# Performance work log

Measured on AMD Instinct MI355X. Metric: run time of the kernel, lower is better.

The kernel has to match this reference:

```python
import jax, jax.numpy as jnp
import numpy as np

D, N, K = 128, 8192, 256


def setup_inputs() -> dict:
    key = jax.random.key(0)
    k1, k2, k3 = jax.random.split(key, 3)
    X = jax.random.normal(k1, (D, N), dtype=jnp.float32)
    N_A = jax.random.normal(k2, (D, D, K), dtype=jnp.float32) / np.sqrt(D)
    N_mu = jax.random.normal(k3, (D, K), dtype=jnp.float32)
    gamma = jnp.float32(-0.01)
    return {"X": X, "N_A": N_A, "N_mu": N_mu, "gamma": gamma}


def reference(X, N_A, N_mu, gamma):
    # N_eval[d,n,c] = sum_e N_A[d,e,c] * (X[e,n] - N_mu[e,c])
    # Split to avoid materializing the (D,D,N,k) broadcast intermediate:
    AX = jnp.einsum('dec,en->dnc', N_A, X)            # (D, N, K)
    Amu = jnp.einsum('dec,ec->dc', N_A, N_mu)          # (D, K)
    N_eval = AX - Amu[:, None, :]                      # (D, N, K)
    sq = jnp.sum(N_eval * N_eval, axis=0)              # (N, K)
    Pi = jax.nn.softmax(gamma * sq, axis=1).T          # (K, N)
    return jnp.vstack((X, Pi))                         # (D+K, N)
```

## Files before the change

kernel.cpp:

```cpp
#include <hip/hip_runtime.h>

#define D_ 128
#define N_ 8192
#define K_ 256

typedef __attribute__((ext_vector_type(4))) float f4;
typedef __attribute__((ext_vector_type(8))) int i8v;
typedef __attribute__((ext_vector_type(4))) int i4v;

__global__ __launch_bounds__(256) void prep_k(
    const float* __restrict__ X, float* __restrict__ out,
    unsigned char* __restrict__ Xf8, const float* __restrict__ NA,
    unsigned char* __restrict__ Af8s, const float* __restrict__ Nmu,
    float* __restrict__ Amut) {
  __shared__ __align__(16) char smem[21568];
  const int t = threadIdx.x;
  const int id = blockIdx.x;

  if (id < 256) {
    float (*tile)[65] = (float (*)[65])smem;
    const int n0 = (id & 127) * 64;
    const int e0 = (id >> 7) * 64;
    const int col = t & 63;
    const int r4 = t >> 6;
    for (int rr = 0; rr < 64; rr += 4) {
      int e = rr + r4;
      float v = X[(size_t)(e0 + e) * N_ + n0 + col];
      tile[e][col] = v;
      out[(size_t)(e0 + e) * N_ + n0 + col] = v;
    }
    __syncthreads();
    const int chunk = t & 15;
    for (int iter = 0; iter < 4; ++iter) {
      int nl = iter * 16 + (t >> 4);
      float v0 = tile[chunk * 4 + 0][nl];
      float v1 = tile[chunk * 4 + 1][nl];
      float v2 = tile[chunk * 4 + 2][nl];
      float v3 = tile[chunk * 4 + 3][nl];
      int pk = __builtin_amdgcn_cvt_pk_fp8_f32(v0, v1, 0, false);
      pk = __builtin_amdgcn_cvt_pk_fp8_f32(v2, v3, pk, true);
      *(int*)&Xf8[(size_t)(n0 + nl) * D_ + e0 + chunk * 4] = pk;
    }
  } else {
    const int aid = id - 256;
    const int dtl = aid & 7;
    const int c0 = (aid >> 3) * 8;
    unsigned char* AT = (unsigned char*)smem;
    float* mu_s = (float*)(smem + 17472);
    {
      const int cl = t & 7;
      const int er = t >> 3;
#pragma unroll
      for (int pass = 0; pass < 4; ++pass) {
        int e = pass * 32 + er;
        mu_s[cl * 128 + e] = Nmu[(size_t)e * K_ + c0 + cl];
      }
    }
    const int c4 = t & 1;
    const int pe = t >> 1;
#pragma unroll 4
    for (int iter = 0; iter < 16; ++iter) {
      int p = iter * 128 + pe;
      int d = p >> 7, e = p & 127;
      float4 v = *(const float4*)&NA[((size_t)(dtl * 16 + d) * D_ + e) * K_ + c0 + c4 * 4];
      int pk0 = __builtin_amdgcn_cvt_pk_fp8_f32(v.x, v.x, 0, false);
      int pk1 = __builtin_amdgcn_cvt_pk_fp8_f32(v.y, v.y, 0, false);
      int pk2 = __builtin_amdgcn_cvt_pk_fp8_f32(v.z, v.z, 0, false);
      int pk3 = __builtin_amdgcn_cvt_pk_fp8_f32(v.w, v.w, 0, false);
      AT[(c4 * 4 + 0) * 2184 + d * 136 + e] = (unsigned char)(pk0 & 0xff);
      AT[(c4 * 4 + 1) * 2184 + d * 136 + e] = (unsigned char)(pk1 & 0xff);
      AT[(c4 * 4 + 2) * 2184 + d * 136 + e] = (unsigned char)(pk2 & 0xff);
      AT[(c4 * 4 + 3) * 2184 + d * 136 + e] = (unsigned char)(pk3 & 0xff);
    }
    __syncthreads();
    if (t < 128) {
      const int d_loc = t >> 3;
      const int cl = t & 7;
      const unsigned char* row = &AT[cl * 2184 + d_loc * 136];
      const float* mr = &mu_s[cl * 128];
      float s = 0.f;
#pragma unroll
      for (int j = 0; j < 16; ++j) {
        int2 v = *(const int2*)(row + j * 8);
        const int e0 = j * 8;
        s += __builtin_amdgcn_cvt_f32_fp8(v.x, 0) * mr[e0 + 0];
        s += __builtin_amdgcn_cvt_f32_fp8(v.x, 1) * mr[e0 + 1];
        s += __builtin_amdgcn_cvt_f32_fp8(v.x, 2) * mr[e0 + 2];
        s += __builtin_amdgcn_cvt_f32_fp8(v.x, 3) * mr[e0 + 3];
        s += __builtin_amdgcn_cvt_f32_fp8(v.y, 0) * mr[e0 + 4];
        s += __builtin_amdgcn_cvt_f32_fp8(v.y, 1) * mr[e0 + 5];
        s += __builtin_amdgcn_cvt_f32_fp8(v.y, 2) * mr[e0 + 6];
        s += __builtin_amdgcn_cvt_f32_fp8(v.y, 3) * mr[e0 + 7];
      }
      Amut[(size_t)(c0 + cl) * D_ + dtl * 16 + d_loc] = -s;
    }
    const int w = t >> 6, L = t & 63, q = L >> 4, m = L & 15;
#pragma unroll
    for (int it = 0; it < 4; ++it) {
      int u = w + it * 4;
      int ucl = u >> 1, h = u & 1;
      const unsigned char* base = AT + ucl * 2184 + m * 136 + q * 32 + h * 16;
      unsigned long long lo = *(const unsigned long long*)(base);
      unsigned long long hi = *(const unsigned long long*)(base + 8);
      ulonglong2 val; val.x = lo; val.y = hi;
      *(ulonglong2*)(Af8s + (size_t)(c0 + ucl) * 16384 + dtl * 2048 + h * 1024 + L * 16) = val;
    }
  }
}

__global__ __launch_bounds__(256, 4) void main_k(
    const unsigned char* __restrict__ Af8s, const unsigned char* __restrict__ Xf8,
    const float* __restrict__ Amut, float* __restrict__ sqws) {
  __shared__ unsigned char A0s[16384];
  __shared__ unsigned char A1s[16384];
  __shared__ float amus[2][D_];
  const int t = threadIdx.x;
  const int w = t >> 6;
  const int L = t & 63;
  const int m = L & 15;
  const int q = L >> 4;

  const int id = blockIdx.x;
  const int xcd = id & 7;
  const int s = id >> 3;
  const int yb = xcd * 4 + (s & 3);
  const int xb = s >> 2;
  const int n0 = xb * 256;
  const int c0 = yb * 8;

  i8v xf[4];
#pragma unroll
  for (int jt = 0; jt < 4; ++jt)
    xf[jt] = *(const i8v*)(Xf8 + (size_t)(n0 + w * 64 + jt * 16 + m) * D_ + q * 32);

  const unsigned char* pl = Af8s + (size_t)c0 * 16384;

#define STAGE(SRC, DST)                                                          \
  {                                                                              \
    _Pragma("unroll")                                                            \
    for (int it_ = 0; it_ < 4; ++it_)                                            \
      __builtin_amdgcn_global_load_lds(                                          \
          (const unsigned int*)((SRC) + (it_ * 256 + t) * 16),                   \
          (unsigned int*)((DST) + (it_ * 256 + w * 64) * 16), 16, 0, 0);         \
  }

  STAGE(pl, A0s);
  if (t < 32)
    __builtin_amdgcn_global_load_lds((const unsigned int*)(Amut + (size_t)c0 * D_ + t * 4),
                                     (unsigned int*)&amus[0][0], 16, 0, 0);

  auto compute = [&](const unsigned char* buf, const float* amurow, int c) {
    float ss0 = 0.f, ss1 = 0.f, ss2 = 0.f, ss3 = 0.f;
#pragma unroll
    for (int dtl = 0; dtl < 8; ++dtl) {
      i4v lo = *(const i4v*)(buf + dtl * 2048 + L * 16);
      i4v hi = *(const i4v*)(buf + dtl * 2048 + 1024 + L * 16);
      i8v a;
      a[0] = lo[0]; a[1] = lo[1]; a[2] = lo[2]; a[3] = lo[3];
      a[4] = hi[0]; a[5] = hi[1]; a[6] = hi[2]; a[7] = hi[3];
      f4 camu = *(const f4*)&amurow[dtl * 16 + q * 4];
#pragma unroll
      for (int jt = 0; jt < 4; ++jt) {
        f4 acc = __builtin_amdgcn_mfma_scale_f32_16x16x128_f8f6f4(
            a, xf[jt], camu, 0, 0, 0, 0x7f7f7f7f, 0, 0x7f7f7f7f);
        float sj = acc[0] * acc[0] + acc[1] * acc[1] + acc[2] * acc[2] + acc[3] * acc[3];
        if (jt == 0) ss0 += sj; else if (jt == 1) ss1 += sj;
        else if (jt == 2) ss2 += sj; else ss3 += sj;
      }
    }
    ss0 += __shfl_xor(ss0, 16, 64);  ss0 += __shfl_xor(ss0, 32, 64);
    ss1 += __shfl_xor(ss1, 16, 64);  ss1 += __shfl_xor(ss1, 32, 64);
    ss2 += __shfl_xor(ss2, 16, 64);  ss2 += __shfl_xor(ss2, 32, 64);
    ss3 += __shfl_xor(ss3, 16, 64);  ss3 += __shfl_xor(ss3, 32, 64);
    float sel = (q == 0) ? ss0 : (q == 1) ? ss1 : (q == 2) ? ss2 : ss3;
    sqws[(size_t)c * N_ + n0 + w * 64 + L] = sel;
  };

  for (int ci2 = 0; ci2 < 4; ++ci2) {
    const int cA = c0 + ci2 * 2;
    __syncthreads();
    STAGE(pl + (size_t)(ci2 * 2 + 1) * 16384, A1s);
    if (t < 32)
      __builtin_amdgcn_global_load_lds(
          (const unsigned int*)(Amut + (size_t)(cA + 1) * D_ + t * 4),
          (unsigned int*)&amus[1][0], 16, 0, 0);
    compute(A0s, &amus[0][0], cA);

    __syncthreads();
    if (ci2 < 3) {
      STAGE(pl + (size_t)(ci2 * 2 + 2) * 16384, A0s);
      if (t < 32)
        __builtin_amdgcn_global_load_lds(
            (const unsigned int*)(Amut + (size_t)(cA + 2) * D_ + t * 4),
            (unsigned int*)&amus[0][0], 16, 0, 0);
    }
    compute(A1s, &amus[1][0], cA + 1);
  }
#undef STAGE
}

__global__ __launch_bounds__(256) void softmax_k(const float* __restrict__ sqws,
                                                 const float* __restrict__ gptr,
                                                 float* __restrict__ out) {
  __shared__ float s_ld[256][36];
  __shared__ float red[8][32];
  __shared__ float red2[8][32];
  const int t = threadIdx.x;
  const int n0 = blockIdx.x * 32;
  const float gamma = *gptr;
#pragma unroll
  for (int it = 0; it < 8; ++it) {
    int f = it * 256 + t;
    int c = f >> 3, nq = f & 7;
    *(float4*)&s_ld[c][nq * 4] = *(const float4*)&sqws[(size_t)c * N_ + n0 + nq * 4];
  }
  __syncthreads();
  const int nl = t & 31;
  const int cg = t >> 5;
  float mxp = -1e30f;
#pragma unroll
  for (int cc = 0; cc < 32; ++cc)
    mxp = fmaxf(mxp, gamma * s_ld[cg * 32 + cc][nl]);
  red[cg][nl] = mxp;
  __syncthreads();
  float mx = red[0][nl];
#pragma unroll
  for (int g2 = 1; g2 < 8; ++g2) mx = fmaxf(mx, red[g2][nl]);
  float ex[32];
  float z = 0.f;
#pragma unroll
  for (int cc = 0; cc < 32; ++cc) {
    ex[cc] = __expf(gamma * s_ld[cg * 32 + cc][nl] - mx);
    z += ex[cc];
  }
  red2[cg][nl] = z;
  __syncthreads();
  float zz = red2[0][nl];
#pragma unroll
  for (int g2 = 1; g2 < 8; ++g2) zz += red2[g2][nl];
  float rz = 1.f / zz;
#pragma unroll
  for (int cc = 0; cc < 32; ++cc)
    out[(size_t)(D_ + cg * 32 + cc) * N_ + n0 + nl] = ex[cc] * rz;
}

extern "C" void kernel_launch(void* const* d_in, const int* in_sizes, int n_in,
                              void* d_out, int out_size, void* d_ws, size_t ws_size,
                              hipStream_t stream) {
  const float* X   = (const float*)d_in[0];
  const float* NA  = (const float*)d_in[1];
  const float* Nmu = (const float*)d_in[2];
  const float* g   = (const float*)d_in[3];
  float* out = (float*)d_out;
  char* ws = (char*)d_ws;

  unsigned char* Xf8  = (unsigned char*)(ws);
  unsigned char* Af8s = (unsigned char*)(ws + 1048576);
  float* Amut         = (float*)(ws + 5242880);
  float* sqws         = (float*)(ws + 5373952);

  hipLaunchKernelGGL(prep_k, dim3(512), dim3(256), 0, stream,
                     X, out, Xf8, NA, Af8s, Nmu, Amut);
  hipLaunchKernelGGL(main_k, dim3(1024), dim3(256), 0, stream,
                     Af8s, Xf8, Amut, sqws);
  hipLaunchKernelGGL(softmax_k, dim3(N_ / 32), dim3(256), 0, stream, sqws, g, out);
}
```

Measured before the change: 114.3 us.

## Switch MFMA operands from FP8 to packed FP6 with custom encoding

Replaces FP8 quantization of X and N_A with a hand-written FP6 (e2m3) encoder. Operands are bit-packed at 6 bits per element, and the MFMA scale instruction runs in FP6 mode. N_A is pre-scaled by 8 and gamma is divided by 64 to compensate. This cuts the workspace and LDS staging bytes for the A planes and X rows, and may allow a faster FP6 MFMA rate. The cost is lower precision with saturation at 7.5, plus extra ALU work for software encoding in the prep kernel.

```diff
diff --git a/kernel.cpp b/kernel.cpp
--- a/kernel.cpp
+++ b/kernel.cpp
@@ -8,10 +8,32 @@
 typedef __attribute__((ext_vector_type(8))) int i8v;
 typedef __attribute__((ext_vector_type(4))) int i4v;
 
+__device__ __forceinline__ int enc6(float v) {
+  unsigned s = (__float_as_uint(v) >> 31) << 5;
+  float a = fminf(fabsf(v), 7.5f);
+  int code;
+  if (a < 2.f) {
+    code = (int)rintf(a * 8.f);
+  } else if (a < 4.f) {
+    code = 16 + ((int)rintf(a * 4.f) - 8);
+  } else {
+    code = 24 + ((int)rintf(a * 2.f) - 8);
+  }
+  return code | (int)s;
+}
+
+__device__ __forceinline__ float dec6(int c) {
+  int M = c & 7, E = (c >> 3) & 3;
+  int mant = (E == 0) ? M : (8 + M);
+  float sc = (E <= 1) ? 0.125f : (E == 2 ? 0.25f : 0.5f);
+  float v = (float)mant * sc;
+  return (c & 32) ? -v : v;
+}
+
 __global__ __launch_bounds__(256) void prep_k(
     const float* __restrict__ X, float* __restrict__ out,
-    unsigned char* __restrict__ Xf8, const float* __restrict__ NA,
-    unsigned char* __restrict__ Af8s, const float* __restrict__ Nmu,
+    unsigned char* __restrict__ Xf6, const float* __restrict__ NA,
+    unsigned char* __restrict__ Af6s, const float* __restrict__ Nmu,
     float* __restrict__ Amut) {
   __shared__ __align__(16) char smem[21568];
   const int t = threadIdx.x;
@@ -30,17 +52,28 @@
       out[(size_t)(e0 + e) * N_ + n0 + col] = v;
     }
     __syncthreads();
-    const int chunk = t & 15;
-    for (int iter = 0; iter < 4; ++iter) {
-      int nl = iter * 16 + (t >> 4);
-      float v0 = tile[chunk * 4 + 0][nl];
-      float v1 = tile[chunk * 4 + 1][nl];
-      float v2 = tile[chunk * 4 + 2][nl];
-      float v3 = tile[chunk * 4 + 3][nl];
-      int pk = __builtin_amdgcn_cvt_pk_fp8_f32(v0, v1, 0, false);
-      pk = __builtin_amdgcn_cvt_pk_fp8_f32(v2, v3, pk, true);
-      *(int*)&Xf8[(size_t)(n0 + nl) * D_ + e0 + chunk * 4] = pk;
-    }
+    const int nl = t >> 2;
+    const int ql = (t >> 1) & 1;
+    const int h = t & 1;
+    unsigned long long lo = 0; unsigned int hi = 0;
+#pragma unroll
+    for (int j = 0; j < 16; ++j) {
+      unsigned long long c = (unsigned long long)enc6(tile[ql * 32 + h * 16 + j][nl]);
+      const int pos = 6 * j;
+      if (pos <= 58) {
+        lo |= c << pos;
+        if (pos == 60) hi |= (unsigned int)(c >> 4);
+      } else if (pos < 64) {
+        lo |= c << pos;
+        hi |= (unsigned int)(c >> (64 - pos));
+      } else {
+        hi |= (unsigned int)(c << (pos - 64));
+      }
+    }
+    unsigned char* dst = Xf6 + (size_t)(n0 + nl) * 128 + (e0 / 32 + ql) * 32 + h * 12;
+    *(unsigned int*)(dst + 0) = (unsigned int)lo;
+    *(unsigned int*)(dst + 4) = (unsigned int)(lo >> 32);
+    *(unsigned int*)(dst + 8) = hi;
   } else {
     const int aid = id - 256;
     const int dtl = aid & 7;
@@ -63,14 +96,10 @@
       int p = iter * 128 + pe;
       int d = p >> 7, e = p & 127;
       float4 v = *(const float4*)&NA[((size_t)(dtl * 16 + d) * D_ + e) * K_ + c0 + c4 * 4];
-      int pk0 = __builtin_amdgcn_cvt_pk_fp8_f32(v.x, v.x, 0, false);
-      int pk1 = __builtin_amdgcn_cvt_pk_fp8_f32(v.y, v.y, 0, false);
-      int pk2 = __builtin_amdgcn_cvt_pk_fp8_f32(v.z, v.z, 0, false);
-      int pk3 = __builtin_amdgcn_cvt_pk_fp8_f32(v.w, v.w, 0, false);
-      AT[(c4 * 4 + 0) * 2184 + d * 136 + e] = (unsigned char)(pk0 & 0xff);
-      AT[(c4 * 4 + 1) * 2184 + d * 136 + e] = (unsigned char)(pk1 & 0xff);
-      AT[(c4 * 4 + 2) * 2184 + d * 136 + e] = (unsigned char)(pk2 & 0xff);
-      AT[(c4 * 4 + 3) * 2184 + d * 136 + e] = (unsigned char)(pk3 & 0xff);
+      AT[(c4 * 4 + 0) * 2184 + d * 136 + e] = (unsigned char)enc6(v.x * 8.f);
+      AT[(c4 * 4 + 1) * 2184 + d * 136 + e] = (unsigned char)enc6(v.y * 8.f);
+      AT[(c4 * 4 + 2) * 2184 + d * 136 + e] = (unsigned char)enc6(v.z * 8.f);
+      AT[(c4 * 4 + 3) * 2184 + d * 136 + e] = (unsigned char)enc6(v.w * 8.f);
     }
     __syncthreads();
     if (t < 128) {
@@ -82,37 +111,59 @@
 #pragma unroll
       for (int j = 0; j < 16; ++j) {
         int2 v = *(const int2*)(row + j * 8);
-        const int e0 = j * 8;
-        s += __builtin_amdgcn_cvt_f32_fp8(v.x, 0) * mr[e0 + 0];
-        s += __builtin_amdgcn_cvt_f32_fp8(v.x, 1) * mr[e0 + 1];
-        s += __builtin_amdgcn_cvt_f32_fp8(v.x, 2) * mr[e0 + 2];
-        s += __builtin_amdgcn_cvt_f32_fp8(v.x, 3) * mr[e0 + 3];
-        s += __builtin_amdgcn_cvt_f32_fp8(v.y, 0) * mr[e0 + 4];
-        s += __builtin_amdgcn_cvt_f32_fp8(v.y, 1) * mr[e0 + 5];
-        s += __builtin_amdgcn_cvt_f32_fp8(v.y, 2) * mr[e0 + 6];
-        s += __builtin_amdgcn_cvt_f32_fp8(v.y, 3) * mr[e0 + 7];
+        const int e0i = j * 8;
+        s += dec6(v.x & 63) * mr[e0i + 0];
+        s += dec6((v.x >> 8) & 63) * mr[e0i + 1];
+        s += dec6((v.x >> 16) & 63) * mr[e0i + 2];
+        s += dec6((v.x >> 24) & 63) * mr[e0i + 3];
+        s += dec6(v.y & 63) * mr[e0i + 4];
+        s += dec6((v.y >> 8) & 63) * mr[e0i + 5];
+        s += dec6((v.y >> 16) & 63) * mr[e0i + 6];
+        s += dec6((v.y >> 24) & 63) * mr[e0i + 7];
       }
       Amut[(size_t)(c0 + cl) * D_ + dtl * 16 + d_loc] = -s;
     }
-    const int w = t >> 6, L = t & 63, q = L >> 4, m = L & 15;
-#pragma unroll
-    for (int it = 0; it < 4; ++it) {
-      int u = w + it * 4;
-      int ucl = u >> 1, h = u & 1;
-      const unsigned char* base = AT + ucl * 2184 + m * 136 + q * 32 + h * 16;
-      unsigned long long lo = *(const unsigned long long*)(base);
-      unsigned long long hi = *(const unsigned long long*)(base + 8);
-      ulonglong2 val; val.x = lo; val.y = hi;
-      *(ulonglong2*)(Af8s + (size_t)(c0 + ucl) * 16384 + dtl * 2048 + h * 1024 + L * 16) = val;
+#pragma unroll
+    for (int r = 0; r < 2; ++r) {
+      const int task = r * 256 + t;
+      const int cl = task >> 6;
+      const int L = task & 63;
+      const unsigned char* cp = AT + cl * 2184 + (L & 15) * 136 + (L >> 4) * 32;
+      unsigned long long w0 = 0, w1 = 0, w2 = 0;
+#pragma unroll
+      for (int g = 0; g < 4; ++g) {
+        int2 dv = *(const int2*)(cp + g * 8);
+#pragma unroll
+        for (int half = 0; half < 2; ++half) {
+          unsigned int d = (half == 0) ? (unsigned int)dv.x : (unsigned int)dv.y;
+          unsigned long long g24 =
+              (unsigned long long)((d & 63u) | ((d >> 8) & 63u) << 6 |
+                                   ((d >> 16) & 63u) << 12 | ((d >> 24) & 63u) << 18);
+          const int pos = (g * 2 + half) * 24;
+          if (pos < 64) {
+            w0 |= g24 << pos;
+            if (pos > 40) w1 |= g24 >> (64 - pos);
+          } else if (pos < 128) {
+            w1 |= g24 << (pos - 64);
+            if (pos - 64 > 40) w2 |= g24 >> (128 - pos);
+          } else {
+            w2 |= g24 << (pos - 128);
+          }
+        }
+      }
+      unsigned char* plane = Af6s + (size_t)(c0 + cl) * 12288;
+      ulonglong2 val; val.x = w0; val.y = w1;
+      *(ulonglong2*)(plane + dtl * 1024 + L * 16) = val;
+      *(unsigned long long*)(plane + 8192 + dtl * 512 + L * 8) = w2;
     }
   }
 }
 
 __global__ __launch_bounds__(256, 4) void main_k(
-    const unsigned char* __restrict__ Af8s, const unsigned char* __restrict__ Xf8,
+    const unsigned char* __restrict__ Af6s, const unsigned char* __restrict__ Xf6,
     const float* __restrict__ Amut, float* __restrict__ sqws) {
-  __shared__ unsigned char A0s[16384];
-  __shared__ unsigned char A1s[16384];
+  __shared__ unsigned char A0s[12288];
+  __shared__ unsigned char A1s[12288];
   __shared__ float amus[2][D_];
   const int t = threadIdx.x;
   const int w = t >> 6;
@@ -130,15 +181,22 @@
 
   i8v xf[4];
 #pragma unroll
-  for (int jt = 0; jt < 4; ++jt)
-    xf[jt] = *(const i8v*)(Xf8 + (size_t)(n0 + w * 64 + jt * 16 + m) * D_ + q * 32);
-
-  const unsigned char* pl = Af8s + (size_t)c0 * 16384;
+  for (int jt = 0; jt < 4; ++jt) {
+    const unsigned char* xr = Xf6 + (size_t)(n0 + w * 64 + jt * 16 + m) * 128 + q * 32;
+    i4v x0 = *(const i4v*)(xr);
+    int2 x1 = *(const int2*)(xr + 16);
+    i8v f;
+    f[0] = x0[0]; f[1] = x0[1]; f[2] = x0[2]; f[3] = x0[3];
+    f[4] = x1.x;  f[5] = x1.y;  f[6] = 0;     f[7] = 0;
+    xf[jt] = f;
+  }
+
+  const unsigned char* pl = Af6s + (size_t)c0 * 12288;
 
 #define STAGE(SRC, DST)                                                          \
   {                                                                              \
     _Pragma("unroll")                                                            \
-    for (int it_ = 0; it_ < 4; ++it_)                                            \
+    for (int it_ = 0; it_ < 3; ++it_)                                            \
       __builtin_amdgcn_global_load_lds(                                          \
           (const unsigned int*)((SRC) + (it_ * 256 + t) * 16),                   \
           (unsigned int*)((DST) + (it_ * 256 + w * 64) * 16), 16, 0, 0);         \
@@ -153,16 +211,16 @@
     float ss0 = 0.f, ss1 = 0.f, ss2 = 0.f, ss3 = 0.f;
 #pragma unroll
     for (int dtl = 0; dtl < 8; ++dtl) {
-      i4v lo = *(const i4v*)(buf + dtl * 2048 + L * 16);
-      i4v hi = *(const i4v*)(buf + dtl * 2048 + 1024 + L * 16);
+      i4v p0 = *(const i4v*)(buf + dtl * 1024 + L * 16);
+      int2 p1 = *(const int2*)(buf + 8192 + dtl * 512 + L * 8);
       i8v a;
-      a[0] = lo[0]; a[1] = lo[1]; a[2] = lo[2]; a[3] = lo[3];
-      a[4] = hi[0]; a[5] = hi[1]; a[6] = hi[2]; a[7] = hi[3];
+      a[0] = p0[0]; a[1] = p0[1]; a[2] = p0[2]; a[3] = p0[3];
+      a[4] = p1.x;  a[5] = p1.y;  a[6] = 0;     a[7] = 0;
       f4 camu = *(const f4*)&amurow[dtl * 16 + q * 4];
 #pragma unroll
       for (int jt = 0; jt < 4; ++jt) {
         f4 acc = __builtin_amdgcn_mfma_scale_f32_16x16x128_f8f6f4(
-            a, xf[jt], camu, 0, 0, 0, 0x7f7f7f7f, 0, 0x7f7f7f7f);
+            a, xf[jt], camu, 2, 2, 0, 0x7f7f7f7f, 0, 0x7f7f7f7f);
         float sj = acc[0] * acc[0] + acc[1] * acc[1] + acc[2] * acc[2] + acc[3] * acc[3];
         if (jt == 0) ss0 += sj; else if (jt == 1) ss1 += sj;
         else if (jt == 2) ss2 += sj; else ss3 += sj;
@@ -179,7 +237,7 @@
   for (int ci2 = 0; ci2 < 4; ++ci2) {
     const int cA = c0 + ci2 * 2;
     __syncthreads();
-    STAGE(pl + (size_t)(ci2 * 2 + 1) * 16384, A1s);
+    STAGE(pl + (size_t)(ci2 * 2 + 1) * 12288, A1s);
     if (t < 32)
       __builtin_amdgcn_global_load_lds(
           (const unsigned int*)(Amut + (size_t)(cA + 1) * D_ + t * 4),
@@ -188,7 +246,7 @@
 
     __syncthreads();
     if (ci2 < 3) {
-      STAGE(pl + (size_t)(ci2 * 2 + 2) * 16384, A0s);
+      STAGE(pl + (size_t)(ci2 * 2 + 2) * 12288, A0s);
       if (t < 32)
         __builtin_amdgcn_global_load_lds(
             (const unsigned int*)(Amut + (size_t)(cA + 2) * D_ + t * 4),
@@ -207,7 +265,7 @@
   __shared__ float red2[8][32];
   const int t = threadIdx.x;
   const int n0 = blockIdx.x * 32;
-  const float gamma = *gptr;
+  const float gamma = *gptr * 0.015625f;
 #pragma unroll
   for (int it = 0; it < 8; ++it) {
     int f = it * 256 + t;
@@ -254,14 +312,14 @@
   float* out = (float*)d_out;
   char* ws = (char*)d_ws;
 
-  unsigned char* Xf8  = (unsigned char*)(ws);
-  unsigned char* Af8s = (unsigned char*)(ws + 1048576);
+  unsigned char* Xf6  = (unsigned char*)(ws);
+  unsigned char* Af6s = (unsigned char*)(ws + 1048576);
   float* Amut         = (float*)(ws + 5242880);
   float* sqws         = (float*)(ws + 5373952);
 
   hipLaunchKernelGGL(prep_k, dim3(512), dim3(256), 0, stream,
-                     X, out, Xf8, NA, Af8s, Nmu, Amut);
+                     X, out, Xf6, NA, Af6s, Nmu, Amut);
   hipLaunchKernelGGL(main_k, dim3(1024), dim3(256), 0, stream,
-                     Af8s, Xf8, Amut, sqws);
+                     Af6s, Xf6, Amut, sqws);
   hipLaunchKernelGGL(softmax_k, dim3(N_ / 32), dim3(256), 0, stream, sqws, g, out);
 }
```

Measured after the change: 116.1 us. Within noise of the previous version (+1.6%).
